# Performance work log

Measured on AMD Instinct MI355X. Metric: run time of the kernel, lower is better.

Reference implementation:

```python
import jax, jax.numpy as jnp
import numpy as np

H = 16  # num_heads
LN_EPS = 1e-5


def setup_inputs() -> dict:
    key = jax.random.key(0)
    ks = jax.random.split(key, 9)
    B, Lq, Lkv, D = 8, 512, 1024, 1024
    s = 1.0 / np.sqrt(D)
    return {
        "query": jax.random.normal(ks[0], (B, Lq, D), dtype=jnp.float32),
        "key": jax.random.normal(ks[1], (B, Lkv, D), dtype=jnp.float32),
        "value": jax.random.normal(ks[2], (B, Lkv, D), dtype=jnp.float32),
        "in_proj_w": jax.random.normal(ks[3], (3 * D, D), dtype=jnp.float32) * s,
        "in_proj_b": jnp.zeros((3 * D,), dtype=jnp.float32),
        "out_proj_w": jax.random.normal(ks[4], (D, D), dtype=jnp.float32) * s,
        "out_proj_b": jnp.zeros((D,), dtype=jnp.float32),
        "ln_gamma": jnp.ones((D,), dtype=jnp.float32),
        "ln_beta": jnp.zeros((D,), dtype=jnp.float32),
    }


def reference(query, key, value, in_proj_w, in_proj_b, out_proj_w, out_proj_b, ln_gamma, ln_beta):
    B, Lq, D = query.shape
    Lkv = key.shape[1]
    hd = D // H
    wq, wk, wv = jnp.split(in_proj_w, 3, axis=0)   # each [D, D]
    bq, bk, bv = jnp.split(in_proj_b, 3, axis=0)

    def heads(x, L):
        return x.reshape(B, L, H, hd).transpose(0, 2, 1, 3)  # [B,H,L,hd]

    q = heads(query @ wq.T + bq, Lq) * (1.0 / np.sqrt(hd))
    k = heads(key @ wk.T + bk, Lkv)
    v = heads(value @ wv.T + bv, Lkv)

    scores = jnp.einsum('bhqd,bhkd->bhqk', q, k)           # [B,H,Lq,Lkv]
    attn = jax.nn.softmax(scores, axis=-1)
    # attention dropout: identity in eval mode
    ctx = jnp.einsum('bhqk,bhkd->bhqd', attn, v)           # [B,H,Lq,hd]
    ctx = ctx.transpose(0, 2, 1, 3).reshape(B, Lq, D)
    attn_out = ctx @ out_proj_w.T + out_proj_b

    # residual dropout: identity in eval mode; then LayerNorm
    x = query + attn_out
    mu = jnp.mean(x, axis=-1, keepdims=True)
    var = jnp.mean(jnp.square(x - mu), axis=-1, keepdims=True)
    output = (x - mu) * jax.lax.rsqrt(var + LN_EPS) * ln_gamma + ln_beta

    attn_weights = attn.mean(axis=1)                        # avg over heads [B,Lq,Lkv]
    return (output, attn_weights)
```

## Files before the change

### kernel.cpp

```cpp
#include <hip/hip_runtime.h>
#include <stdint.h>

typedef __attribute__((ext_vector_type(8))) short short8;
typedef __attribute__((ext_vector_type(4))) float f32x4;

#define DEV static __device__ __forceinline__

DEV unsigned short f2bf(float f) {
    union { float f; unsigned int u; } v; v.f = f;
    unsigned int u = v.u;
    return (unsigned short)((u + 0x7fffu + ((u >> 16) & 1u)) >> 16);
}

DEV float bf2f(unsigned short s) {
    union { unsigned int u; float f; } v; v.u = ((unsigned int)s) << 16;
    return v.f;
}

DEV void async_lds16(const void* g, void* l) {
    __builtin_amdgcn_global_load_lds(
        (const __attribute__((address_space(1))) unsigned int*)g,
        (__attribute__((address_space(3))) unsigned int*)l, 16, 0, 0);
}

__global__ void k_cvt(const float* __restrict__ in, unsigned short* __restrict__ out, int n4) {
    int i = blockIdx.x * blockDim.x + threadIdx.x;
    int stride = gridDim.x * blockDim.x;
    for (; i < n4; i += stride) {
        float4 v = ((const float4*)in)[i];
        ushort4 o;
        o.x = f2bf(v.x); o.y = f2bf(v.y); o.z = f2bf(v.z); o.w = f2bf(v.w);
        ((ushort4*)out)[i] = o;
    }
}

template<int EPI>
__global__ __launch_bounds__(256)
void k_gemm(const unsigned short* __restrict__ A,
            const unsigned short* __restrict__ Bm,
            const float* __restrict__ bias,
            const float* __restrict__ resid,
            void* __restrict__ Cout)
{
    __shared__ unsigned short As[128 * 64];
    __shared__ unsigned short Bs[128 * 64];
    const int t = threadIdx.x;
    const int lane = t & 63, w = t >> 6;
    const int i16 = lane & 15, g = lane >> 4;
    const int wr = w >> 1, wc = w & 1;
    const int row0 = blockIdx.x * 128;
    const int col0 = blockIdx.y * 128;
    const int K = 1024;

    f32x4 acc[4][4];
#pragma unroll
    for (int a = 0; a < 4; ++a)
#pragma unroll
        for (int b = 0; b < 4; ++b) acc[a][b] = f32x4{0.f, 0.f, 0.f, 0.f};

    for (int kt = 0; kt < K / 64; ++kt) {
        const unsigned short* Ag = A + (size_t)row0 * K + kt * 64;
        const unsigned short* Bg = Bm + (size_t)col0 * K + kt * 64;
#pragma unroll
        for (int s = 0; s < 4; ++s) {
            int ch = s * 256 + t;
            int r = ch >> 3, cb = (ch & 7) * 8;
            async_lds16(Ag + (size_t)r * K + cb, &As[ch * 8]);
            async_lds16(Bg + (size_t)r * K + cb, &Bs[ch * 8]);
        }
        __syncthreads();
#pragma unroll
        for (int ks = 0; ks < 2; ++ks) {
            short8 af[4], bfr[4];
#pragma unroll
            for (int mi = 0; mi < 4; ++mi)
                af[mi] = *(const short8*)&As[(wr * 64 + mi * 16 + i16) * 64 + ks * 32 + g * 8];
#pragma unroll
            for (int ni = 0; ni < 4; ++ni)
                bfr[ni] = *(const short8*)&Bs[(wc * 64 + ni * 16 + i16) * 64 + ks * 32 + g * 8];
#pragma unroll
            for (int mi = 0; mi < 4; ++mi)
#pragma unroll
                for (int ni = 0; ni < 4; ++ni)
                    acc[mi][ni] = __builtin_amdgcn_mfma_f32_16x16x32_bf16(af[mi], bfr[ni], acc[mi][ni], 0, 0, 0);
        }
        __syncthreads();
    }

#pragma unroll
    for (int mi = 0; mi < 4; ++mi) {
#pragma unroll
        for (int ni = 0; ni < 4; ++ni) {
#pragma unroll
            for (int r = 0; r < 4; ++r) {
                int row = row0 + wr * 64 + mi * 16 + g * 4 + r;
                int col = col0 + wc * 64 + ni * 16 + i16;
                float v = acc[mi][ni][r] + bias[col];
                if (EPI == 0) {
                    ((unsigned short*)Cout)[(size_t)row * 1024 + col] = f2bf(v * 0.125f);
                } else if (EPI == 1) {
                    int b = row >> 10, kv = row & 1023, h = col >> 6, d = col & 63;
                    ((unsigned short*)Cout)[((size_t)(b * 16 + h) * 1024 + kv) * 64 + d] = f2bf(v);
                } else if (EPI == 2) {
                    int b = row >> 10, kv = row & 1023, h = col >> 6, d = col & 63;
                    ((unsigned short*)Cout)[((size_t)(b * 16 + h) * 64 + d) * 1024 + kv] = f2bf(v);
                } else {
                    ((float*)Cout)[(size_t)row * 1024 + col] = v + resid[(size_t)row * 1024 + col];
                }
            }
        }
    }
}

__global__ __launch_bounds__(512)
void k_attn(const unsigned short* __restrict__ qf,
            const unsigned short* __restrict__ kh,
            const unsigned short* __restrict__ vt,
            unsigned short* __restrict__ ctx,
            unsigned short* __restrict__ attw_part)
{
    __shared__ unsigned short q_lds[16 * 256];
    __shared__ unsigned short p_lds[16 * 1032];
    __shared__ float ctxbuf[16][68];
    __shared__ float redsum[8][16];
    __shared__ float gsum[16];

    const int t = threadIdx.x;
    const int lane = t & 63, w = t >> 6;
    const int i16 = lane & 15, g = lane >> 4;
    const int bid = blockIdx.x;
    const int logical = (bid & 7) * 128 + (bid >> 3);
    const int qt = logical & 31;
    const int bh = logical >> 5;
    const int b = bh >> 2, hg = bh & 3;
    const int q0 = qt * 16;
    const int wn = w & 3, khf = w >> 2;

    {
        const unsigned short* qg = qf + ((size_t)(b * 512 + q0)) * 1024 + hg * 256;
        int q = t >> 5, c = t & 31;
        int sc = (c * 8) ^ ((q & 7) << 3);
        async_lds16(qg + (size_t)q * 1024 + sc, &q_lds[t * 8]);
    }
    __syncthreads();

    float attw_acc[8][4];
#pragma unroll
    for (int mt = 0; mt < 8; ++mt)
#pragma unroll
        for (int r = 0; r < 4; ++r) attw_acc[mt][r] = 0.f;

    for (int hh = 0; hh < 4; ++hh) {
        const int h = hg * 4 + hh;
        short8 qb0, qb1;
        {
            int sw = (i16 & 7) << 4;
            const char* qb = (const char*)q_lds + i16 * 512;
            qb0 = *(const short8*)(qb + ((hh * 128 + g * 16) ^ sw));
            qb1 = *(const short8*)(qb + ((hh * 128 + 64 + g * 16) ^ sw));
        }
        const unsigned short* khb = kh + (size_t)(b * 16 + h) * 1024 * 64;
        f32x4 c[8];
#pragma unroll
        for (int mt = 0; mt < 8; ++mt) c[mt] = f32x4{0.f, 0.f, 0.f, 0.f};
#pragma unroll
        for (int mt = 0; mt < 8; ++mt) {
            const unsigned short* kp = khb + (size_t)(w * 128 + mt * 16 + i16) * 64 + g * 8;
            short8 a0 = *(const short8*)kp;
            short8 a1 = *(const short8*)(kp + 32);
            c[mt] = __builtin_amdgcn_mfma_f32_16x16x32_bf16(a0, qb0, c[mt], 0, 0, 0);
            c[mt] = __builtin_amdgcn_mfma_f32_16x16x32_bf16(a1, qb1, c[mt], 0, 0, 0);
        }
        float s = 0.f;
#pragma unroll
        for (int mt = 0; mt < 8; ++mt)
#pragma unroll
            for (int r = 0; r < 4; ++r) {
                float ev = __expf(c[mt][r]);
                c[mt][r] = ev;
                s += ev;
            }
        s += __shfl_xor(s, 16);
        s += __shfl_xor(s, 32);
        if (lane < 16) redsum[w][lane] = s;
#pragma unroll
        for (int mt = 0; mt < 8; ++mt) {
            unsigned int lo = (unsigned int)f2bf(c[mt][0]) | ((unsigned int)f2bf(c[mt][1]) << 16);
            unsigned int hi = (unsigned int)f2bf(c[mt][2]) | ((unsigned int)f2bf(c[mt][3]) << 16);
            uint2 pk; pk.x = lo; pk.y = hi;
            int kv = w * 128 + mt * 16 + g * 4;
            *(uint2*)&p_lds[(size_t)i16 * 1032 + kv] = pk;
        }
        __syncthreads();
        float gs = 0.f;
#pragma unroll
        for (int ww = 0; ww < 8; ++ww) gs += redsum[ww][i16];
        if (w == 0 && lane < 16) gsum[lane] = gs;
        float rs16 = 0.0625f / gs;
#pragma unroll
        for (int mt = 0; mt < 8; ++mt)
#pragma unroll
            for (int r = 0; r < 4; ++r) attw_acc[mt][r] += c[mt][r] * rs16;
        f32x4 cc = f32x4{0.f, 0.f, 0.f, 0.f};
        const unsigned short* vb = vt + ((size_t)(b * 16 + h) * 64 + wn * 16 + i16) * 1024 + khf * 512 + g * 8;
        const unsigned short* pb = &p_lds[(size_t)i16 * 1032 + khf * 512 + g * 8];
#pragma unroll
        for (int kt = 0; kt < 16; ++kt) {
            short8 pa = *(const short8*)(pb + kt * 32);
            short8 vv = *(const short8*)(vb + kt * 32);
            cc = __builtin_amdgcn_mfma_f32_16x16x32_bf16(pa, vv, cc, 0, 0, 0);
        }
        if (khf == 0) {
#pragma unroll
            for (int r = 0; r < 4; ++r) ctxbuf[g * 4 + r][wn * 16 + i16] = cc[r];
        }
        __syncthreads();
        if (khf == 1) {
#pragma unroll
            for (int r = 0; r < 4; ++r) {
                int q = g * 4 + r;
                float v = cc[r] + ctxbuf[q][wn * 16 + i16];
                ctx[((size_t)b * 512 + q0 + q) * 1024 + h * 64 + wn * 16 + i16] = f2bf(v / gsum[q]);
            }
        }
        __syncthreads();
    }

    unsigned short* pw = attw_part + (size_t)hg * (8u * 512u * 1024u)
                       + ((size_t)(b * 512 + q0 + i16)) * 1024;
#pragma unroll
    for (int mt = 0; mt < 8; ++mt) {
        ushort4 o;
        o.x = f2bf(attw_acc[mt][0]); o.y = f2bf(attw_acc[mt][1]);
        o.z = f2bf(attw_acc[mt][2]); o.w = f2bf(attw_acc[mt][3]);
        int kv = w * 128 + mt * 16 + g * 4;
        *(ushort4*)&pw[kv] = o;
    }
}

__global__ __launch_bounds__(256)
void k_attw_red(const unsigned short* __restrict__ part, float* __restrict__ attw) {
    const size_t GSTRIDE = (size_t)8 * 512 * 1024;
    int n4 = (int)(GSTRIDE / 4);
    int i = blockIdx.x * 256 + threadIdx.x;
    int stride = gridDim.x * 256;
    for (; i < n4; i += stride) {
        float4 acc = {0.f, 0.f, 0.f, 0.f};
#pragma unroll
        for (int gp = 0; gp < 4; ++gp) {
            ushort4 u = ((const ushort4*)(part + gp * GSTRIDE))[i];
            acc.x += bf2f(u.x); acc.y += bf2f(u.y);
            acc.z += bf2f(u.z); acc.w += bf2f(u.w);
        }
        ((float4*)attw)[i] = acc;
    }
}

__global__ __launch_bounds__(256)
void k_ln(const float* __restrict__ x, const float* __restrict__ gamma,
          const float* __restrict__ beta, float* __restrict__ out)
{
    int row = blockIdx.x;
    const float* xr = x + (size_t)row * 1024;
    int t = threadIdx.x;
    float4 v = ((const float4*)xr)[t];
    float s = v.x + v.y + v.z + v.w;
    float sq = v.x * v.x + v.y * v.y + v.z * v.z + v.w * v.w;
#pragma unroll
    for (int o = 32; o > 0; o >>= 1) { s += __shfl_xor(s, o); sq += __shfl_xor(sq, o); }
    __shared__ float rs[4], rq[4];
    int w = t >> 6;
    if ((t & 63) == 0) { rs[w] = s; rq[w] = sq; }
    __syncthreads();
    s = rs[0] + rs[1] + rs[2] + rs[3];
    sq = rq[0] + rq[1] + rq[2] + rq[3];
    float mu = s * (1.f / 1024.f);
    float var = sq * (1.f / 1024.f) - mu * mu;
    float rstd = rsqrtf(var + 1e-5f);
    float4 gm = ((const float4*)gamma)[t];
    float4 bt = ((const float4*)beta)[t];
    float4 o;
    o.x = (v.x - mu) * rstd * gm.x + bt.x;
    o.y = (v.y - mu) * rstd * gm.y + bt.y;
    o.z = (v.z - mu) * rstd * gm.z + bt.z;
    o.w = (v.w - mu) * rstd * gm.w + bt.w;
    ((float4*)(out + (size_t)row * 1024))[t] = o;
}

extern "C" void kernel_launch(void* const* d_in, const int* in_sizes, int n_in,
                              void* d_out, int out_size, void* d_ws, size_t ws_size,
                              hipStream_t stream) {
    const float* query = (const float*)d_in[0];
    const float* key   = (const float*)d_in[1];
    const float* value = (const float*)d_in[2];
    const float* inw   = (const float*)d_in[3];
    const float* inb   = (const float*)d_in[4];
    const float* outw  = (const float*)d_in[5];
    const float* outb  = (const float*)d_in[6];
    const float* lng   = (const float*)d_in[7];
    const float* lnb   = (const float*)d_in[8];

    char* ws = (char*)d_ws;
    unsigned short* query_bf = (unsigned short*)(ws);
    unsigned short* key_bf   = (unsigned short*)(ws + ((size_t)8 << 20));
    unsigned short* value_bf = (unsigned short*)(ws + ((size_t)24 << 20));
    unsigned short* inw_bf   = (unsigned short*)(ws + ((size_t)40 << 20));
    unsigned short* outw_bf  = (unsigned short*)(ws + ((size_t)46 << 20));
    unsigned short* q_flat   = (unsigned short*)(ws + ((size_t)48 << 20));
    unsigned short* k_heads  = (unsigned short*)(ws + ((size_t)56 << 20));
    unsigned short* vt_heads = (unsigned short*)(ws + ((size_t)72 << 20));
    unsigned short* ctx_bf   = query_bf;
    unsigned short* attw_part= key_bf;
    float*          x_f32    = (float*)(ws + ((size_t)24 << 20));

    float* out0 = (float*)d_out;
    float* attw = out0 + (size_t)4096 * 1024;

    k_cvt<<<dim3(1024), dim3(256), 0, stream>>>(query, query_bf, (4096 * 1024) / 4);
    k_cvt<<<dim3(1024), dim3(256), 0, stream>>>(key, key_bf, (8192 * 1024) / 4);
    k_cvt<<<dim3(1024), dim3(256), 0, stream>>>(value, value_bf, (8192 * 1024) / 4);
    k_cvt<<<dim3(1024), dim3(256), 0, stream>>>(inw, inw_bf, (3 * 1024 * 1024) / 4);
    k_cvt<<<dim3(512), dim3(256), 0, stream>>>(outw, outw_bf, (1024 * 1024) / 4);

    k_gemm<0><<<dim3(32, 8), dim3(256), 0, stream>>>(query_bf, inw_bf, inb, nullptr, q_flat);
    k_gemm<1><<<dim3(64, 8), dim3(256), 0, stream>>>(key_bf, inw_bf + (size_t)1024 * 1024, inb + 1024, nullptr, k_heads);
    k_gemm<2><<<dim3(64, 8), dim3(256), 0, stream>>>(value_bf, inw_bf + (size_t)2 * 1024 * 1024, inb + 2048, nullptr, vt_heads);

    k_attn<<<dim3(1024), dim3(512), 0, stream>>>(q_flat, k_heads, vt_heads, ctx_bf, attw_part);
    k_attw_red<<<dim3(2048), dim3(256), 0, stream>>>(attw_part, attw);

    k_gemm<3><<<dim3(32, 8), dim3(256), 0, stream>>>(ctx_bf, outw_bf, outb, query, x_f32);
    k_ln<<<dim3(4096), dim3(256), 0, stream>>>(x_f32, lng, lnb, out0);
}
```

Measured before the change: 405.6 us.

## Store K/V projections in MFMA-fragment tiled layout and swizzle P in LDS

The K and V projection epilogues now write in a layout tiled to match the MFMA operand fragments, so each lane's 16-byte fragment load in the attention kernel comes from a contiguous block rather than a strided row. The padded P buffer in LDS is replaced by an XOR-swizzled layout to avoid bank conflicts without extra memory. The PV loop uses two independent accumulators to expose more MFMA parallelism. The trailing barrier per head is dropped, which depends on the remaining barriers still ordering all shared-buffer reuse. Some unused leftover variables remain.

Result: faster. 350.8 us (-13.5%).

```diff
diff --git a/kernel.cpp b/kernel.cpp
--- a/kernel.cpp
+++ b/kernel.cpp
@@ -99,11 +99,17 @@
                 if (EPI == 0) {
                     ((unsigned short*)Cout)[(size_t)row * 1024 + col] = f2bf(v * 0.125f);
                 } else if (EPI == 1) {
-                    int b = row >> 10, kv = row & 1023, h = col >> 6, d = col & 63;
-                    ((unsigned short*)Cout)[((size_t)(b * 16 + h) * 1024 + kv) * 64 + d] = f2bf(v);
+                    int bb = row >> 10, kv = row & 1023, h = col >> 6, d = col & 63;
+                    size_t addr = (size_t)(bb * 16 + h) * 65536
+                                + (size_t)(kv >> 4) * 1024 + (d >> 5) * 512
+                                + ((d >> 3) & 3) * 128 + (kv & 15) * 8 + (d & 7);
+                    ((unsigned short*)Cout)[addr] = f2bf(v);
                 } else if (EPI == 2) {
-                    int b = row >> 10, kv = row & 1023, h = col >> 6, d = col & 63;
-                    ((unsigned short*)Cout)[((size_t)(b * 16 + h) * 64 + d) * 1024 + kv] = f2bf(v);
+                    int bb = row >> 10, kv = row & 1023, h = col >> 6, d = col & 63;
+                    size_t addr = (size_t)(bb * 16 + h) * 65536
+                                + (size_t)(kv >> 5) * 2048 + ((kv >> 3) & 3) * 512
+                                + (d >> 4) * 128 + (d & 15) * 8 + (kv & 7);
+                    ((unsigned short*)Cout)[addr] = f2bf(v);
                 } else {
                     ((float*)Cout)[(size_t)row * 1024 + col] = v + resid[(size_t)row * 1024 + col];
                 }
@@ -120,7 +126,7 @@
             unsigned short* __restrict__ attw_part)
 {
     __shared__ unsigned short q_lds[16 * 256];
-    __shared__ unsigned short p_lds[16 * 1032];
+    __shared__ unsigned short p_lds[16 * 1024];
     __shared__ float ctxbuf[16][68];
     __shared__ float redsum[8][16];
     __shared__ float gsum[16];
@@ -159,15 +165,15 @@
             qb0 = *(const short8*)(qb + ((hh * 128 + g * 16) ^ sw));
             qb1 = *(const short8*)(qb + ((hh * 128 + 64 + g * 16) ^ sw));
         }
-        const unsigned short* khb = kh + (size_t)(b * 16 + h) * 1024 * 64;
+        const unsigned short* kbase = kh + (size_t)(b * 16 + h) * 65536
+                                    + (size_t)w * 8192 + g * 128 + i16 * 8;
         f32x4 c[8];
 #pragma unroll
         for (int mt = 0; mt < 8; ++mt) c[mt] = f32x4{0.f, 0.f, 0.f, 0.f};
 #pragma unroll
         for (int mt = 0; mt < 8; ++mt) {
-            const unsigned short* kp = khb + (size_t)(w * 128 + mt * 16 + i16) * 64 + g * 8;
-            short8 a0 = *(const short8*)kp;
-            short8 a1 = *(const short8*)(kp + 32);
+            short8 a0 = *(const short8*)(kbase + mt * 1024);
+            short8 a1 = *(const short8*)(kbase + mt * 1024 + 512);
             c[mt] = __builtin_amdgcn_mfma_f32_16x16x32_bf16(a0, qb0, c[mt], 0, 0, 0);
             c[mt] = __builtin_amdgcn_mfma_f32_16x16x32_bf16(a1, qb1, c[mt], 0, 0, 0);
         }
@@ -188,8 +194,8 @@
             unsigned int lo = (unsigned int)f2bf(c[mt][0]) | ((unsigned int)f2bf(c[mt][1]) << 16);
             unsigned int hi = (unsigned int)f2bf(c[mt][2]) | ((unsigned int)f2bf(c[mt][3]) << 16);
             uint2 pk; pk.x = lo; pk.y = hi;
-            int kv = w * 128 + mt * 16 + g * 4;
-            *(uint2*)&p_lds[(size_t)i16 * 1032 + kv] = pk;
+            int pwb = (i16 * 2048 + w * 256 + mt * 32 + g * 8) ^ ((i16 & 7) << 4);
+            *(uint2*)((char*)p_lds + pwb) = pk;
         }
         __syncthreads();
         float gs = 0.f;
@@ -201,29 +207,38 @@
         for (int mt = 0; mt < 8; ++mt)
 #pragma unroll
             for (int r = 0; r < 4; ++r) attw_acc[mt][r] += c[mt][r] * rs16;
-        f32x4 cc = f32x4{0.f, 0.f, 0.f, 0.f};
-        const unsigned short* vb = vt + ((size_t)(b * 16 + h) * 64 + wn * 16 + i16) * 1024 + khf * 512 + g * 8;
-        const unsigned short* pb = &p_lds[(size_t)i16 * 1032 + khf * 512 + g * 8];
-#pragma unroll
-        for (int kt = 0; kt < 16; ++kt) {
-            short8 pa = *(const short8*)(pb + kt * 32);
-            short8 vv = *(const short8*)(vb + kt * 32);
-            cc = __builtin_amdgcn_mfma_f32_16x16x32_bf16(pa, vv, cc, 0, 0, 0);
-        }
+        const unsigned short* vbase = vt + (size_t)(b * 16 + h) * 65536
+                                    + (size_t)khf * 32768 + g * 512 + wn * 128 + i16 * 8;
+        f32x4 cc0 = f32x4{0.f, 0.f, 0.f, 0.f};
+        f32x4 cc1 = f32x4{0.f, 0.f, 0.f, 0.f};
+        const char* pbase = (const char*)p_lds + khf * 1024;
+#pragma unroll
+        for (int kt = 0; kt < 16; kt += 2) {
+            int pb0 = (i16 * 2048 + (khf * 1024 + kt * 64 + g * 16) % 2048);
+            (void)pb0;
+            short8 pa0 = *(const short8*)((const char*)p_lds
+                          + ((i16 * 2048 + khf * 1024 + kt * 64 + g * 16) ^ ((i16 & 7) << 4)));
+            short8 vv0 = *(const short8*)(vbase + kt * 2048);
+            cc0 = __builtin_amdgcn_mfma_f32_16x16x32_bf16(pa0, vv0, cc0, 0, 0, 0);
+            short8 pa1 = *(const short8*)((const char*)p_lds
+                          + ((i16 * 2048 + khf * 1024 + (kt + 1) * 64 + g * 16) ^ ((i16 & 7) << 4)));
+            short8 vv1 = *(const short8*)(vbase + (kt + 1) * 2048);
+            cc1 = __builtin_amdgcn_mfma_f32_16x16x32_bf16(pa1, vv1, cc1, 0, 0, 0);
+        }
+        (void)pbase;
         if (khf == 0) {
 #pragma unroll
-            for (int r = 0; r < 4; ++r) ctxbuf[g * 4 + r][wn * 16 + i16] = cc[r];
+            for (int r = 0; r < 4; ++r) ctxbuf[g * 4 + r][wn * 16 + i16] = cc0[r] + cc1[r];
         }
         __syncthreads();
         if (khf == 1) {
 #pragma unroll
             for (int r = 0; r < 4; ++r) {
                 int q = g * 4 + r;
-                float v = cc[r] + ctxbuf[q][wn * 16 + i16];
+                float v = cc0[r] + cc1[r] + ctxbuf[q][wn * 16 + i16];
                 ctx[((size_t)b * 512 + q0 + q) * 1024 + h * 64 + wn * 16 + i16] = f2bf(v / gsum[q]);
             }
         }
-        __syncthreads();
     }
 
     unsigned short* pw = attw_part + (size_t)hg * (8u * 512u * 1024u)
```
